# Optimization experiments

Measured on AMD Instinct MI355X. Metric: run time of the kernel, lower is better.

## Reference

```python
import jax, jax.numpy as jnp
import numpy as np

N = 100000   # nodes
E = 1600000  # edges (avg degree 16)
IN, H, OUT = 128, 128, 64
EPS = 1e-5


def setup_inputs() -> dict:
    key = jax.random.key(0)
    ks = jax.random.split(key, 8)

    def glorot(k, i, o):
        s = 1.0 / np.sqrt(i)
        return jax.random.uniform(k, (i, o), jnp.float32, -s, s)

    return {
        "x": jax.random.normal(ks[0], (N, IN), jnp.float32),
        "edge_index": jax.random.randint(ks[1], (2, E), 0, N, dtype=jnp.int32),
        "W1": glorot(ks[2], IN, H), "b1": jnp.zeros((H,), jnp.float32),
        "g1": jnp.ones((H,), jnp.float32), "be1": jnp.zeros((H,), jnp.float32),
        "W2": glorot(ks[3], H, H), "b2": jnp.zeros((H,), jnp.float32),
        "g2": jnp.ones((H,), jnp.float32), "be2": jnp.zeros((H,), jnp.float32),
        "W3": glorot(ks[4], H, OUT), "b3": jnp.zeros((OUT,), jnp.float32),
    }


def gcn_conv(x, W, b, src, dst):
    # PyG GCNConv: add self-loops, symmetric norm D^-1/2 (A+I) D^-1/2, then x@W, bias after aggregation.
    n = x.shape[0]
    h = x @ W                                   # [N, out]
    deg = jnp.zeros((n,), h.dtype).at[dst].add(1.0) + 1.0  # +1 for self-loop
    dis = jax.lax.rsqrt(deg)                    # deg^-1/2
    coef = dis[src] * dis[dst]                  # per-edge norm
    agg = jnp.zeros_like(h).at[dst].add(h[src] * coef[:, None])
    agg = agg + h * (dis * dis)[:, None]        # self-loop messages
    return agg + b


def batch_norm(x, g, b):
    # BatchNorm1d in training mode: batch statistics over nodes, biased variance.
    m = x.mean(axis=0)
    v = x.var(axis=0)
    return (x - m) * jax.lax.rsqrt(v + EPS) * g + b


def reference(x, edge_index, W1, b1, g1, be1, W2, b2, g2, be2, W3, b3):
    src, dst = edge_index[0], edge_index[1]
    h = gcn_conv(x, W1, b1, src, dst)
    h = batch_norm(h, g1, be1)
    h = gcn_conv(h, W2, b2, src, dst)
    h = batch_norm(h, g2, be2)
    out = gcn_conv(h, W3, b3, src, dst)
    return out
```

## Files before the change

### kernel.cpp

```cpp
#include <hip/hip_runtime.h>
#include <hip/hip_fp16.h>


constexpr int BSH = 7;
constexpr int NXCD = 8;

typedef _Float16 half8 __attribute__((ext_vector_type(8)));
typedef float f32x4 __attribute__((ext_vector_type(4)));

static __device__ inline ushort f2h(float f) {
    union { __half h; ushort u; } cv;
    cv.h = __float2half_rn(f);
    return cv.u;
}
static __device__ inline float2 h2f2(unsigned int u) {
    union { unsigned int u; __half2 h; } cv;
    cv.u = u;
    return __half22float2(cv.h);
}

#define ACC8(v) do { float2 _f; \
    _f = h2f2((v).x); acc[0] += _f.x; acc[1] += _f.y; \
    _f = h2f2((v).y); acc[2] += _f.x; acc[3] += _f.y; \
    _f = h2f2((v).z); acc[4] += _f.x; acc[5] += _f.y; \
    _f = h2f2((v).w); acc[6] += _f.x; acc[7] += _f.y; \
} while (0)

__global__ __launch_bounds__(256) void count_k(const int* __restrict__ dst,
                                               int* __restrict__ hist,
                                               int E, int EPB, int nbuk) {
    __shared__ int lh[1024];
    for (int i = threadIdx.x; i < nbuk; i += 256) lh[i] = 0;
    __syncthreads();
    const int e0 = blockIdx.x * EPB;
    const int e1 = min(e0 + EPB, E);
    for (int e = e0 + threadIdx.x; e < e1; e += 256)
        atomicAdd(&lh[dst[e] >> BSH], 1);
    __syncthreads();
    const int xcd = blockIdx.x & (NXCD - 1);
    for (int i = threadIdx.x; i < nbuk; i += 256) {
        int v = lh[i];
        if (v) atomicAdd(&hist[xcd * nbuk + i], v);
    }
}

__global__ __launch_bounds__(256) void scan_hist_k(const int* __restrict__ hist,
                                                   int* __restrict__ cur,
                                                   int* __restrict__ bstart,
                                                   int* __restrict__ row_ptr,
                                                   float* __restrict__ stats,
                                                   int nbuk, int n, int E) {
    stats[threadIdx.x] = 0.f;
    const int NT = nbuk * NXCD;
    const int C = (NT + 255) / 256;
    int vals[32];
    const int tid = threadIdx.x;
    int sum = 0;
#pragma unroll
    for (int k = 0; k < 32; ++k) {
        if (k >= C) break;
        int key = tid * C + k;
        int v = 0;
        if (key < NT) {
            int b = key >> 3, x = key & 7;
            v = hist[x * nbuk + b];
        }
        vals[k] = v;
        sum += v;
    }
    __shared__ int part[256];
    part[tid] = sum;
    __syncthreads();
    for (int off = 1; off < 256; off <<= 1) {
        int t = 0;
        if (tid >= off) t = part[tid - off];
        __syncthreads();
        part[tid] += t;
        __syncthreads();
    }
    int run = (tid == 0) ? 0 : part[tid - 1];
#pragma unroll
    for (int k = 0; k < 32; ++k) {
        if (k >= C) break;
        int key = tid * C + k;
        if (key < NT) {
            int b = key >> 3, x = key & 7;
            cur[x * nbuk + b] = run;
            if (x == 0) bstart[b] = run;
        }
        run += vals[k];
    }
    if (tid == 0) { bstart[nbuk] = E; row_ptr[n] = E; }
}

__global__ __launch_bounds__(256) void scatter_bucket_k(const int* __restrict__ src,
                                                        const int* __restrict__ dst,
                                                        int* __restrict__ cur,
                                                        unsigned int* __restrict__ ebuf,
                                                        int E, int EPB, int nbuk) {
    __shared__ int lh[1024];
    __shared__ int base[1024];
    for (int i = threadIdx.x; i < nbuk; i += 256) lh[i] = 0;
    __syncthreads();
    const int e0 = blockIdx.x * EPB;
    const int e1 = min(e0 + EPB, E);
    const int xcd = blockIdx.x & (NXCD - 1);
    for (int e = e0 + threadIdx.x; e < e1; e += 256)
        atomicAdd(&lh[dst[e] >> BSH], 1);
    __syncthreads();
    for (int i = threadIdx.x; i < nbuk; i += 256) {
        int v = lh[i];
        base[i] = v ? atomicAdd(&cur[xcd * nbuk + i], v) : 0;
        lh[i] = 0;
    }
    __syncthreads();
    for (int e = e0 + threadIdx.x; e < e1; e += 256) {
        int d = dst[e];
        int s = src[e];
        int b = d >> BSH;
        int pos = base[b] + atomicAdd(&lh[b], 1);
        ebuf[pos] = ((unsigned int)s << BSH) | (unsigned int)(d & 127);
    }
}

__global__ __launch_bounds__(256) void bucket_sort_k(const unsigned int* __restrict__ ebuf,
                                                     const int* __restrict__ bstart,
                                                     int* __restrict__ row_ptr,
                                                     int* __restrict__ esrc, int n) {
    const int b = blockIdx.x;
    const int beg = bstart[b];
    const int end = bstart[b + 1];
    __shared__ int cnt[128], off[128];
    if (threadIdx.x < 128) cnt[threadIdx.x] = 0;
    __syncthreads();
    for (int i = beg + threadIdx.x; i < end; i += 256)
        atomicAdd(&cnt[ebuf[i] & 127], 1);
    __syncthreads();
    if (threadIdx.x < 128) off[threadIdx.x] = cnt[threadIdx.x];
    __syncthreads();
    for (int d = 1; d < 128; d <<= 1) {
        int t = 0;
        if (threadIdx.x < 128 && threadIdx.x >= d) t = off[threadIdx.x - d];
        __syncthreads();
        if (threadIdx.x < 128) off[threadIdx.x] += t;
        __syncthreads();
    }
    if (threadIdx.x < 128) {
        int ex = off[threadIdx.x] - cnt[threadIdx.x];
        int node = (b << BSH) + threadIdx.x;
        if (node < n) row_ptr[node] = beg + ex;
        cnt[threadIdx.x] = ex;
    }
    __syncthreads();
    for (int i = beg + threadIdx.x; i < end; i += 256) {
        unsigned int p = ebuf[i];
        int l = (int)(p & 127);
        int pos = beg + atomicAdd(&cnt[l], 1);
        esrc[pos] = (int)(p >> BSH);
    }
}

__global__ void rowptr_to_dis_k(const int* __restrict__ row_ptr,
                                float* __restrict__ dis, int n) {
    int i = blockIdx.x * blockDim.x + threadIdx.x;
    if (i < n) {
        int deg = row_ptr[i + 1] - row_ptr[i];
        dis[i] = rsqrtf((float)deg + 1.0f);
    }
}

__global__ __launch_bounds__(256) void prep_wt_k(const float* __restrict__ W1,
                                                 const float* __restrict__ W2,
                                                 const float* __restrict__ W3,
                                                 ushort* __restrict__ wt1,
                                                 ushort* __restrict__ wt2,
                                                 ushort* __restrict__ wt3) {
    const float* W; ushort* WT; int OUTD;
    if (blockIdx.x == 0)      { W = W1; WT = wt1; OUTD = 128; }
    else if (blockIdx.x == 1) { W = W2; WT = wt2; OUTD = 128; }
    else                      { W = W3; WT = wt3; OUTD = 64; }
    const int tot = 128 * OUTD;
    for (int idx = threadIdx.x; idx < tot; idx += 256) {
        int nq = idx >> 7;
        int k  = idx & 127;
        WT[idx] = f2h(W[k * OUTD + nq]);
    }
}

template <int OUTD, bool XF16, bool BNIN>
__global__ __launch_bounds__(256) void gemm_reg_k(const void* __restrict__ Xv,
                                                  const ushort* __restrict__ WT,
                                                  const float* __restrict__ scale,
                                                  const float* __restrict__ shift,
                                                  const float* __restrict__ dis,
                                                  ushort* __restrict__ Hs, int nn) {
    constexpr int NCT = OUTD / 16;
    const int wave = threadIdx.x >> 6;
    const int lane = threadIdx.x & 63;
    const int l15 = lane & 15;
    const int kg = lane >> 4;
    const int row = blockIdx.x * 64 + wave * 16 + l15;

    half8 a[4];
#pragma unroll
    for (int kk = 0; kk < 4; ++kk) {
        float v[8];
        if (row < nn) {
            if (XF16) {
                const uint4* xp = (const uint4*)((const ushort*)Xv + (size_t)row * 128
                                                 + kk * 32 + kg * 8);
                uint4 raw = *xp;
                float2 f;
                f = h2f2(raw.x); v[0] = f.x; v[1] = f.y;
                f = h2f2(raw.y); v[2] = f.x; v[3] = f.y;
                f = h2f2(raw.z); v[4] = f.x; v[5] = f.y;
                f = h2f2(raw.w); v[6] = f.x; v[7] = f.y;
            } else {
                const float4* xp = (const float4*)((const float*)Xv + (size_t)row * 128
                                                   + kk * 32 + kg * 8);
                float4 v0 = xp[0];
                float4 v1 = xp[1];
                v[0] = v0.x; v[1] = v0.y; v[2] = v0.z; v[3] = v0.w;
                v[4] = v1.x; v[5] = v1.y; v[6] = v1.z; v[7] = v1.w;
            }
            if (BNIN) {
                int kq = kk * 8 + kg * 2;
                float4 s0 = ((const float4*)scale)[kq];
                float4 s1 = ((const float4*)scale)[kq + 1];
                float4 h0 = ((const float4*)shift)[kq];
                float4 h1 = ((const float4*)shift)[kq + 1];
                v[0] = v[0] * s0.x + h0.x;
                v[1] = v[1] * s0.y + h0.y;
                v[2] = v[2] * s0.z + h0.z;
                v[3] = v[3] * s0.w + h0.w;
                v[4] = v[4] * s1.x + h1.x;
                v[5] = v[5] * s1.y + h1.y;
                v[6] = v[6] * s1.z + h1.z;
                v[7] = v[7] * s1.w + h1.w;
            }
#pragma unroll
            for (int j = 0; j < 8; ++j) a[kk][j] = (_Float16)v[j];
        } else {
#pragma unroll
            for (int j = 0; j < 8; ++j) a[kk][j] = (_Float16)0.f;
        }
    }

    f32x4 acc[NCT];
#pragma unroll
    for (int ct = 0; ct < NCT; ++ct) acc[ct] = (f32x4){0.f, 0.f, 0.f, 0.f};

#pragma unroll
    for (int kk = 0; kk < 4; ++kk) {
#pragma unroll
        for (int ct = 0; ct < NCT; ++ct) {
            half8 bfr = *(const half8*)&WT[(ct * 16 + l15) * 128 + kk * 32 + kg * 8];
            acc[ct] = __builtin_amdgcn_mfma_f32_16x16x32_f16(a[kk], bfr, acc[ct], 0, 0, 0);
        }
    }

    const int mbase = blockIdx.x * 64 + wave * 16 + kg * 4;
    float dm[4];
#pragma unroll
    for (int reg = 0; reg < 4; ++reg) {
        int m = mbase + reg;
        dm[reg] = (m < nn) ? dis[m] : 0.f;
    }
#pragma unroll
    for (int ct = 0; ct < NCT; ++ct) {
        int ncol = ct * 16 + l15;
        size_t cb = (size_t)(ncol >> 5) * nn * 32 + (ncol & 31);
#pragma unroll
        for (int reg = 0; reg < 4; ++reg) {
            int m = mbase + reg;
            if (m < nn) Hs[cb + (size_t)m * 32] = f2h(acc[ct][reg] * dm[reg]);
        }
    }
}

template <int OUTD, bool STATS, bool OUTF16>
__global__ __launch_bounds__(256) void gather_k(const ushort* __restrict__ Hs,
                                                const float* __restrict__ dis,
                                                const float* __restrict__ b,
                                                const int* __restrict__ row_ptr,
                                                const int* __restrict__ esrc,
                                                void* __restrict__ Ov,
                                                float* __restrict__ sums,
                                                float* __restrict__ sumsq, int n) {
    constexpr int NCHUNK = OUTD / 32;

    __shared__ float s_sum[32];
    __shared__ float s_sq[32];
    if (STATS) {
        if (threadIdx.x < 32) { s_sum[threadIdx.x] = 0.f; s_sq[threadIdx.x] = 0.f; }
        __syncthreads();
    }

    const int chunk = blockIdx.x & (NCHUNK - 1);
    const int nblk  = blockIdx.x / NCHUNK;
    const int g     = threadIdx.x >> 2;
    const int lane  = threadIdx.x & 3;
    const int node  = nblk * 64 + g;

    float acc[8];
#pragma unroll
    for (int c = 0; c < 8; ++c) acc[c] = 0.f;
    float o[8];
#pragma unroll
    for (int c = 0; c < 8; ++c) o[c] = 0.f;

    if (node < n) {
        const uint4* Hc = (const uint4*)Hs + (size_t)chunk * n * 4;

        {
            uint4 v = Hc[(size_t)node * 4 + lane];
            ACC8(v);
        }
        const int beg = row_ptr[node];
        const int end = row_ptr[node + 1];
        int j = beg;
        const int end8 = beg + ((end - beg) & ~7);
        for (; j < end8; j += 8) {
            int s[8];
#pragma unroll
            for (int u = 0; u < 8; ++u) s[u] = esrc[j + u];
            uint4 va[8];
#pragma unroll
            for (int u = 0; u < 8; ++u) va[u] = Hc[(size_t)s[u] * 4 + lane];
#pragma unroll
            for (int u = 0; u < 8; ++u) { ACC8(va[u]); }
        }
        for (; j < end; ++j) {
            int s = esrc[j];
            uint4 a = Hc[(size_t)s * 4 + lane];
            ACC8(a);
        }

        float dd = dis[node];
        const float4* B4 = (const float4*)b + chunk * 8 + lane * 2;
        float4 b0 = B4[0];
        float4 b1 = B4[1];
        o[0] = acc[0] * dd + b0.x;
        o[1] = acc[1] * dd + b0.y;
        o[2] = acc[2] * dd + b0.z;
        o[3] = acc[3] * dd + b0.w;
        o[4] = acc[4] * dd + b1.x;
        o[5] = acc[5] * dd + b1.y;
        o[6] = acc[6] * dd + b1.z;
        o[7] = acc[7] * dd + b1.w;

        if (OUTF16) {
            union { ushort us[8]; uint4 v; } pk;
#pragma unroll
            for (int c = 0; c < 8; ++c) pk.us[c] = f2h(o[c]);
            ((uint4*)Ov)[(size_t)node * (OUTD / 8) + chunk * 4 + lane] = pk.v;
        } else {
            float4* O4 = (float4*)Ov + (size_t)node * (OUTD / 4) + chunk * 8 + lane * 2;
            O4[0] = make_float4(o[0], o[1], o[2], o[3]);
            O4[1] = make_float4(o[4], o[5], o[6], o[7]);
        }
    }

    if (STATS) {
        float sv[8], qv[8];
#pragma unroll
        for (int c = 0; c < 8; ++c) { sv[c] = o[c]; qv[c] = o[c] * o[c]; }
#pragma unroll
        for (int c = 0; c < 8; ++c) {
#pragma unroll
            for (int m = 4; m <= 32; m <<= 1) {
                sv[c] += __shfl_xor(sv[c], m);
                qv[c] += __shfl_xor(qv[c], m);
            }
        }
        if ((threadIdx.x & 63) < 4) {
            int c0 = lane * 8;
#pragma unroll
            for (int c = 0; c < 8; ++c) {
                atomicAdd(&s_sum[c0 + c], sv[c]);
                atomicAdd(&s_sq[c0 + c], qv[c]);
            }
        }
        __syncthreads();
        if (threadIdx.x < 32) {
            atomicAdd(&sums[chunk * 32 + threadIdx.x], s_sum[threadIdx.x]);
            atomicAdd(&sumsq[chunk * 32 + threadIdx.x], s_sq[threadIdx.x]);
        }
    }
}

__global__ void bn_finalize_k(float* __restrict__ sums, float* __restrict__ sumsq,
                              const float* __restrict__ g, const float* __restrict__ be,
                              float* __restrict__ scale, float* __restrict__ shift, int n) {
    int c = threadIdx.x;
    float inv_n = 1.0f / (float)n;
    float m = sums[c] * inv_n;
    float v = sumsq[c] * inv_n - m * m;
    float sc = rsqrtf(v + 1e-5f) * g[c];
    scale[c] = sc;
    shift[c] = be[c] - m * sc;
    sums[c] = 0.f;
    sumsq[c] = 0.f;
}

extern "C" void kernel_launch(void* const* d_in, const int* in_sizes, int n_in,
                              void* d_out, int out_size, void* d_ws, size_t ws_size,
                              hipStream_t stream) {
    const float* x   = (const float*)d_in[0];
    const int*   ei  = (const int*)d_in[1];
    const float* W1  = (const float*)d_in[2];
    const float* b1  = (const float*)d_in[3];
    const float* g1  = (const float*)d_in[4];
    const float* be1 = (const float*)d_in[5];
    const float* W2  = (const float*)d_in[6];
    const float* b2  = (const float*)d_in[7];
    const float* g2  = (const float*)d_in[8];
    const float* be2 = (const float*)d_in[9];
    const float* W3  = (const float*)d_in[10];
    const float* b3  = (const float*)d_in[11];
    float* out = (float*)d_out;

    const int N = in_sizes[0] / 128;
    const int E = in_sizes[1] / 2;
    const int* src = ei;
    const int* dst = ei + E;
    const int NBUK = (N + 127) >> BSH;

    float* wsp   = (float*)d_ws;
    float* dis   = wsp;
    float* stats = wsp + N;
    ushort* wt1  = (ushort*)(stats + 512);
    ushort* wt2  = wt1 + 128 * 128;
    ushort* wt3  = wt2 + 128 * 128;
    int*   hist   = (int*)(wt3 + 128 * 64);
    int*   cur    = hist + NBUK * NXCD;
    int*   bstart = cur + NBUK * NXCD;
    int*   row_ptr = bstart + NBUK + 1 + 63;
    float* bufA  = (float*)((((uintptr_t)(row_ptr + N + 1)) + 255) & ~(uintptr_t)255);
    float* bufB  = bufA + (size_t)N * 128;
    unsigned int* ebuf = (unsigned int*)(bufB + (size_t)N * 128);
    int*   esrc  = (int*)(ebuf + E);

    ushort* Hs  = (ushort*)bufA;
    ushort* Bf16 = (ushort*)bufB;

    float* sums  = stats;
    float* sumsq = stats + 128;
    float* scale = stats + 256;
    float* shift = stats + 384;

    const int BS = 256;
    dim3 blk(BS);
    const int NB = (N + 255) / 256;
    const int SGRID = 128;
    const int EPB = (E + SGRID - 1) / SGRID;

    hipMemsetAsync(hist, 0, (size_t)NBUK * NXCD * 4, stream);
    prep_wt_k<<<dim3(3), blk, 0, stream>>>(W1, W2, W3, wt1, wt2, wt3);
    count_k<<<dim3(SGRID), blk, 0, stream>>>(dst, hist, E, EPB, NBUK);
    scan_hist_k<<<dim3(1), blk, 0, stream>>>(hist, cur, bstart, row_ptr, stats, NBUK, N, E);
    scatter_bucket_k<<<dim3(SGRID), blk, 0, stream>>>(src, dst, cur, ebuf, E, EPB, NBUK);
    bucket_sort_k<<<dim3(NBUK), blk, 0, stream>>>(ebuf, bstart, row_ptr, esrc, N);
    rowptr_to_dis_k<<<dim3(NB), blk, 0, stream>>>(row_ptr, dis, N);

    const int gemm_grid = (N + 63) / 64;
    const int NBg = (N + 63) / 64;

    gemm_reg_k<128, false, false><<<dim3(gemm_grid), blk, 0, stream>>>(
        x, wt1, nullptr, nullptr, dis, Hs, N);
    gather_k<128, true, true><<<dim3(NBg * 4), blk, 0, stream>>>(
        Hs, dis, b1, row_ptr, esrc, Bf16, sums, sumsq, N);
    bn_finalize_k<<<dim3(1), dim3(128), 0, stream>>>(sums, sumsq, g1, be1, scale, shift, N);

    gemm_reg_k<128, true, true><<<dim3(gemm_grid), blk, 0, stream>>>(
        Bf16, wt2, scale, shift, dis, Hs, N);
    gather_k<128, true, true><<<dim3(NBg * 4), blk, 0, stream>>>(
        Hs, dis, b2, row_ptr, esrc, Bf16, sums, sumsq, N);
    bn_finalize_k<<<dim3(1), dim3(128), 0, stream>>>(sums, sumsq, g2, be2, scale, shift, N);

    gemm_reg_k<64, true, true><<<dim3(gemm_grid), blk, 0, stream>>>(
        Bf16, wt3, scale, shift, dis, Hs, N);
    gather_k<64, false, false><<<dim3(NBg * 2), blk, 0, stream>>>(
        Hs, dis, b3, row_ptr, esrc, out, nullptr, nullptr, N);
}
```

Before: 429.8 us.

## Fuse small setup kernels, fold BN finalize into GEMM, accumulate gathers in fp16

Merges the weight-transpose kernel into the histogram count kernel, computes deg^-1/2 inside the bucket sort, and removes the standalone dis and BN-finalize launches by computing BN scale/shift per block in the GEMM prologue, using separate stat buffers per layer. The gather accumulation switches from fp32 adds to packed fp16 __hadd2, which halves the ALU work per neighbor. This cuts several kernel launches and conversion instructions. The fp16 accumulation of about 17 terms risks precision loss and overflow.

```diff
diff --git a/kernel.cpp b/kernel.cpp
--- a/kernel.cpp
+++ b/kernel.cpp
@@ -18,26 +18,51 @@
     cv.u = u;
     return __half22float2(cv.h);
 }
-
-#define ACC8(v) do { float2 _f; \
-    _f = h2f2((v).x); acc[0] += _f.x; acc[1] += _f.y; \
-    _f = h2f2((v).y); acc[2] += _f.x; acc[3] += _f.y; \
-    _f = h2f2((v).z); acc[4] += _f.x; acc[5] += _f.y; \
-    _f = h2f2((v).w); acc[6] += _f.x; acc[7] += _f.y; \
+static __device__ inline __half2 u2h2(unsigned int u) {
+    union { unsigned int u; __half2 h; } cv;
+    cv.u = u;
+    return cv.h;
+}
+
+#define ACCPK(v) do { \
+    acch[0] = __hadd2(acch[0], u2h2((v).x)); \
+    acch[1] = __hadd2(acch[1], u2h2((v).y)); \
+    acch[2] = __hadd2(acch[2], u2h2((v).z)); \
+    acch[3] = __hadd2(acch[3], u2h2((v).w)); \
 } while (0)
 
-__global__ __launch_bounds__(256) void count_k(const int* __restrict__ dst,
-                                               int* __restrict__ hist,
-                                               int E, int EPB, int nbuk) {
+__global__ __launch_bounds__(256) void countwt_k(const int* __restrict__ dst,
+                                                 int* __restrict__ hist,
+                                                 int E, int EPB, int nbuk,
+                                                 const float* __restrict__ W1,
+                                                 const float* __restrict__ W2,
+                                                 const float* __restrict__ W3,
+                                                 ushort* __restrict__ wt1,
+                                                 ushort* __restrict__ wt2,
+                                                 ushort* __restrict__ wt3) {
+    if (blockIdx.x < 3) {
+        const float* W; ushort* WT; int OUTD;
+        if (blockIdx.x == 0)      { W = W1; WT = wt1; OUTD = 128; }
+        else if (blockIdx.x == 1) { W = W2; WT = wt2; OUTD = 128; }
+        else                      { W = W3; WT = wt3; OUTD = 64; }
+        const int tot = 128 * OUTD;
+        for (int idx = threadIdx.x; idx < tot; idx += 256) {
+            int nq = idx >> 7;
+            int k  = idx & 127;
+            WT[idx] = f2h(W[k * OUTD + nq]);
+        }
+        return;
+    }
+    const int bid = blockIdx.x - 3;
     __shared__ int lh[1024];
     for (int i = threadIdx.x; i < nbuk; i += 256) lh[i] = 0;
     __syncthreads();
-    const int e0 = blockIdx.x * EPB;
+    const int e0 = bid * EPB;
     const int e1 = min(e0 + EPB, E);
     for (int e = e0 + threadIdx.x; e < e1; e += 256)
         atomicAdd(&lh[dst[e] >> BSH], 1);
     __syncthreads();
-    const int xcd = blockIdx.x & (NXCD - 1);
+    const int xcd = bid & (NXCD - 1);
     for (int i = threadIdx.x; i < nbuk; i += 256) {
         int v = lh[i];
         if (v) atomicAdd(&hist[xcd * nbuk + i], v);
@@ -51,6 +76,7 @@
                                                    float* __restrict__ stats,
                                                    int nbuk, int n, int E) {
     stats[threadIdx.x] = 0.f;
+    stats[threadIdx.x + 256] = 0.f;
     const int NT = nbuk * NXCD;
     const int C = (NT + 255) / 256;
     int vals[32];
@@ -126,7 +152,8 @@
 __global__ __launch_bounds__(256) void bucket_sort_k(const unsigned int* __restrict__ ebuf,
                                                      const int* __restrict__ bstart,
                                                      int* __restrict__ row_ptr,
-                                                     int* __restrict__ esrc, int n) {
+                                                     int* __restrict__ esrc,
+                                                     float* __restrict__ dis, int n) {
     const int b = blockIdx.x;
     const int beg = bstart[b];
     const int end = bstart[b + 1];
@@ -146,9 +173,13 @@
         __syncthreads();
     }
     if (threadIdx.x < 128) {
-        int ex = off[threadIdx.x] - cnt[threadIdx.x];
+        int deg = cnt[threadIdx.x];
+        int ex = off[threadIdx.x] - deg;
         int node = (b << BSH) + threadIdx.x;
-        if (node < n) row_ptr[node] = beg + ex;
+        if (node < n) {
+            row_ptr[node] = beg + ex;
+            dis[node] = rsqrtf((float)deg + 1.0f);
+        }
         cnt[threadIdx.x] = ex;
     }
     __syncthreads();
@@ -160,41 +191,30 @@
     }
 }
 
-__global__ void rowptr_to_dis_k(const int* __restrict__ row_ptr,
-                                float* __restrict__ dis, int n) {
-    int i = blockIdx.x * blockDim.x + threadIdx.x;
-    if (i < n) {
-        int deg = row_ptr[i + 1] - row_ptr[i];
-        dis[i] = rsqrtf((float)deg + 1.0f);
-    }
-}
-
-__global__ __launch_bounds__(256) void prep_wt_k(const float* __restrict__ W1,
-                                                 const float* __restrict__ W2,
-                                                 const float* __restrict__ W3,
-                                                 ushort* __restrict__ wt1,
-                                                 ushort* __restrict__ wt2,
-                                                 ushort* __restrict__ wt3) {
-    const float* W; ushort* WT; int OUTD;
-    if (blockIdx.x == 0)      { W = W1; WT = wt1; OUTD = 128; }
-    else if (blockIdx.x == 1) { W = W2; WT = wt2; OUTD = 128; }
-    else                      { W = W3; WT = wt3; OUTD = 64; }
-    const int tot = 128 * OUTD;
-    for (int idx = threadIdx.x; idx < tot; idx += 256) {
-        int nq = idx >> 7;
-        int k  = idx & 127;
-        WT[idx] = f2h(W[k * OUTD + nq]);
-    }
-}
-
 template <int OUTD, bool XF16, bool BNIN>
 __global__ __launch_bounds__(256) void gemm_reg_k(const void* __restrict__ Xv,
                                                   const ushort* __restrict__ WT,
-                                                  const float* __restrict__ scale,
-                                                  const float* __restrict__ shift,
+                                                  const float* __restrict__ sums,
+                                                  const float* __restrict__ gg,
+                                                  const float* __restrict__ be,
                                                   const float* __restrict__ dis,
                                                   ushort* __restrict__ Hs, int nn) {
     constexpr int NCT = OUTD / 16;
+    __shared__ __align__(16) float s_scale[BNIN ? 128 : 4];
+    __shared__ __align__(16) float s_shift[BNIN ? 128 : 4];
+    if (BNIN) {
+        if (threadIdx.x < 128) {
+            int c = threadIdx.x;
+            float inv_n = 1.0f / (float)nn;
+            float m = sums[c] * inv_n;
+            float v = sums[c + 128] * inv_n - m * m;
+            float sc = rsqrtf(v + 1e-5f) * gg[c];
+            s_scale[c] = sc;
+            s_shift[c] = be[c] - m * sc;
+        }
+        __syncthreads();
+    }
+
     const int wave = threadIdx.x >> 6;
     const int lane = threadIdx.x & 63;
     const int l15 = lane & 15;
@@ -225,10 +245,10 @@
             }
             if (BNIN) {
                 int kq = kk * 8 + kg * 2;
-                float4 s0 = ((const float4*)scale)[kq];
-                float4 s1 = ((const float4*)scale)[kq + 1];
-                float4 h0 = ((const float4*)shift)[kq];
-                float4 h1 = ((const float4*)shift)[kq + 1];
+                float4 s0 = ((const float4*)s_scale)[kq];
+                float4 s1 = ((const float4*)s_scale)[kq + 1];
+                float4 h0 = ((const float4*)s_shift)[kq];
+                float4 h1 = ((const float4*)s_shift)[kq + 1];
                 v[0] = v[0] * s0.x + h0.x;
                 v[1] = v[1] * s0.y + h0.y;
                 v[2] = v[2] * s0.z + h0.z;
@@ -302,9 +322,9 @@
     const int lane  = threadIdx.x & 3;
     const int node  = nblk * 64 + g;
 
-    float acc[8];
-#pragma unroll
-    for (int c = 0; c < 8; ++c) acc[c] = 0.f;
+    __half2 acch[4];
+#pragma unroll
+    for (int c = 0; c < 4; ++c) acch[c] = __half2(__float2half_rn(0.f), __float2half_rn(0.f));
     float o[8];
 #pragma unroll
     for (int c = 0; c < 8; ++c) o[c] = 0.f;
@@ -314,7 +334,7 @@
 
         {
             uint4 v = Hc[(size_t)node * 4 + lane];
-            ACC8(v);
+            ACCPK(v);
         }
         const int beg = row_ptr[node];
         const int end = row_ptr[node + 1];
@@ -328,26 +348,30 @@
 #pragma unroll
             for (int u = 0; u < 8; ++u) va[u] = Hc[(size_t)s[u] * 4 + lane];
 #pragma unroll
-            for (int u = 0; u < 8; ++u) { ACC8(va[u]); }
+            for (int u = 0; u < 8; ++u) { ACCPK(va[u]); }
         }
         for (; j < end; ++j) {
             int s = esrc[j];
             uint4 a = Hc[(size_t)s * 4 + lane];
-            ACC8(a);
+            ACCPK(a);
         }
 
         float dd = dis[node];
         const float4* B4 = (const float4*)b + chunk * 8 + lane * 2;
         float4 b0 = B4[0];
         float4 b1 = B4[1];
-        o[0] = acc[0] * dd + b0.x;
-        o[1] = acc[1] * dd + b0.y;
-        o[2] = acc[2] * dd + b0.z;
-        o[3] = acc[3] * dd + b0.w;
-        o[4] = acc[4] * dd + b1.x;
-        o[5] = acc[5] * dd + b1.y;
-        o[6] = acc[6] * dd + b1.z;
-        o[7] = acc[7] * dd + b1.w;
+        float2 f0 = __half22float2(acch[0]);
+        float2 f1 = __half22float2(acch[1]);
+        float2 f2 = __half22float2(acch[2]);
+        float2 f3 = __half22float2(acch[3]);
+        o[0] = f0.x * dd + b0.x;
+        o[1] = f0.y * dd + b0.y;
+        o[2] = f1.x * dd + b0.z;
+        o[3] = f1.y * dd + b0.w;
+        o[4] = f2.x * dd + b1.x;
+        o[5] = f2.y * dd + b1.y;
+        o[6] = f3.x * dd + b1.z;
+        o[7] = f3.y * dd + b1.w;
 
         if (OUTF16) {
             union { ushort us[8]; uint4 v; } pk;
@@ -387,20 +411,6 @@
             atomicAdd(&sumsq[chunk * 32 + threadIdx.x], s_sq[threadIdx.x]);
         }
     }
-}
-
-__global__ void bn_finalize_k(float* __restrict__ sums, float* __restrict__ sumsq,
-                              const float* __restrict__ g, const float* __restrict__ be,
-                              float* __restrict__ scale, float* __restrict__ shift, int n) {
-    int c = threadIdx.x;
-    float inv_n = 1.0f / (float)n;
-    float m = sums[c] * inv_n;
-    float v = sumsq[c] * inv_n - m * m;
-    float sc = rsqrtf(v + 1e-5f) * g[c];
-    scale[c] = sc;
-    shift[c] = be[c] - m * sc;
-    sums[c] = 0.f;
-    sumsq[c] = 0.f;
 }
 
 extern "C" void kernel_launch(void* const* d_in, const int* in_sizes, int n_in,
@@ -444,42 +454,36 @@
     ushort* Hs  = (ushort*)bufA;
     ushort* Bf16 = (ushort*)bufB;
 
-    float* sums  = stats;
-    float* sumsq = stats + 128;
-    float* scale = stats + 256;
-    float* shift = stats + 384;
+    float* statsA = stats;
+    float* statsB = stats + 256;
 
     const int BS = 256;
     dim3 blk(BS);
-    const int NB = (N + 255) / 256;
     const int SGRID = 128;
     const int EPB = (E + SGRID - 1) / SGRID;
 
     hipMemsetAsync(hist, 0, (size_t)NBUK * NXCD * 4, stream);
-    prep_wt_k<<<dim3(3), blk, 0, stream>>>(W1, W2, W3, wt1, wt2, wt3);
-    count_k<<<dim3(SGRID), blk, 0, stream>>>(dst, hist, E, EPB, NBUK);
+    countwt_k<<<dim3(SGRID + 3), blk, 0, stream>>>(dst, hist, E, EPB, NBUK,
+                                                   W1, W2, W3, wt1, wt2, wt3);
     scan_hist_k<<<dim3(1), blk, 0, stream>>>(hist, cur, bstart, row_ptr, stats, NBUK, N, E);
     scatter_bucket_k<<<dim3(SGRID), blk, 0, stream>>>(src, dst, cur, ebuf, E, EPB, NBUK);
-    bucket_sort_k<<<dim3(NBUK), blk, 0, stream>>>(ebuf, bstart, row_ptr, esrc, N);
-    rowptr_to_dis_k<<<dim3(NB), blk, 0, stream>>>(row_ptr, dis, N);
+    bucket_sort_k<<<dim3(NBUK), blk, 0, stream>>>(ebuf, bstart, row_ptr, esrc, dis, N);
 
     const int gemm_grid = (N + 63) / 64;
     const int NBg = (N + 63) / 64;
 
     gemm_reg_k<128, false, false><<<dim3(gemm_grid), blk, 0, stream>>>(
-        x, wt1, nullptr, nullptr, dis, Hs, N);
+        x, wt1, nullptr, nullptr, nullptr, dis, Hs, N);
     gather_k<128, true, true><<<dim3(NBg * 4), blk, 0, stream>>>(
-        Hs, dis, b1, row_ptr, esrc, Bf16, sums, sumsq, N);
-    bn_finalize_k<<<dim3(1), dim3(128), 0, stream>>>(sums, sumsq, g1, be1, scale, shift, N);
+        Hs, dis, b1, row_ptr, esrc, Bf16, statsA, statsA + 128, N);
 
     gemm_reg_k<128, true, true><<<dim3(gemm_grid), blk, 0, stream>>>(
-        Bf16, wt2, scale, shift, dis, Hs, N);
+        Bf16, wt2, statsA, g1, be1, dis, Hs, N);
     gather_k<128, true, true><<<dim3(NBg * 4), blk, 0, stream>>>(
-        Hs, dis, b2, row_ptr, esrc, Bf16, sums, sumsq, N);
-    bn_finalize_k<<<dim3(1), dim3(128), 0, stream>>>(sums, sumsq, g2, be2, scale, shift, N);
+        Hs, dis, b2, row_ptr, esrc, Bf16, statsB, statsB + 128, N);
 
     gemm_reg_k<64, true, true><<<dim3(gemm_grid), blk, 0, stream>>>(
-        Bf16, wt3, scale, shift, dis, Hs, N);
+        Bf16, wt3, statsB, g2, be2, dis, Hs, N);
     gather_k<64, false, false><<<dim3(NBg * 2), blk, 0, stream>>>(
         Hs, dis, b3, row_ptr, esrc, out, nullptr, nullptr, N);
 }
```

New measurement: 404.7 us (median of 2 runs). 5.8% less time.
